# Kernel tuning notes

Hardware: AMD Instinct MI355X
Metric: run time of the kernel (lower is better)

The kernel has to match this reference:

```python
import jax, jax.numpy as jnp
import numpy as np

H = 32        # query heads
KV = 8        # key/value heads
D = 128       # head_dim
GROUPS = H // KV
THETA = 10000.0


def _rope_cos_sin(position_ids):
    # position_ids: [B, S] int
    inv_freq = 1.0 / (THETA ** (jnp.arange(0, D, 2, dtype=jnp.float32) / D))  # [D/2]
    freqs = position_ids.astype(jnp.float32)[:, :, None] * inv_freq[None, None, :]  # [B,S,D/2]
    emb = jnp.concatenate([freqs, freqs], axis=-1)  # [B,S,D]
    return jnp.cos(emb), jnp.sin(emb)


def _rotate_half(x):
    x1, x2 = jnp.split(x, 2, axis=-1)
    return jnp.concatenate([-x2, x1], axis=-1)


def _apply_rope(x, cos, sin):
    # x: [B,h,S,D]; cos/sin: [B,S,D] -> broadcast over heads
    return x * cos[:, None, :, :] + _rotate_half(x) * sin[:, None, :, :]


def setup_inputs() -> dict:
    key = jax.random.key(0)
    ks = jax.random.split(key, 8)
    B, S, Dm = 2, 2048, 4096
    scale = lambda d: 1.0 / np.sqrt(d)
    hidden_states = jax.random.normal(ks[0], (B, S, Dm), dtype=jnp.float32)
    position_ids = jnp.broadcast_to(jnp.arange(S, dtype=jnp.int32)[None, :], (B, S))
    Wq = jax.random.normal(ks[1], (Dm, H * D), dtype=jnp.float32) * scale(Dm)
    Wk = jax.random.normal(ks[2], (Dm, KV * D), dtype=jnp.float32) * scale(Dm)
    Wv = jax.random.normal(ks[3], (Dm, KV * D), dtype=jnp.float32) * scale(Dm)
    Wo = jax.random.normal(ks[4], (H * D, Dm), dtype=jnp.float32) * scale(H * D)
    # per-head shift-encoder correction weights (small init so it's a correction)
    Ws_q = jax.random.normal(ks[5], (H, D, D), dtype=jnp.float32) * (0.02 * scale(D))
    Ws_k = jax.random.normal(ks[6], (H, D, D), dtype=jnp.float32) * (0.02 * scale(D))
    return {"hidden_states": hidden_states, "position_ids": position_ids,
            "Wq": Wq, "Wk": Wk, "Wv": Wv, "Wo": Wo, "Ws_q": Ws_q, "Ws_k": Ws_k}


def reference(hidden_states, position_ids, Wq, Wk, Wv, Wo, Ws_q, Ws_k):
    B, S, Dm = hidden_states.shape
    # projections -> [B, heads, S, D]
    q = (hidden_states @ Wq).reshape(B, S, H, D).transpose(0, 2, 1, 3)
    k = (hidden_states @ Wk).reshape(B, S, KV, D).transpose(0, 2, 1, 3)
    v = (hidden_states @ Wv).reshape(B, S, KV, D).transpose(0, 2, 1, 3)
    # RoPE
    cos, sin = _rope_cos_sin(position_ids)
    q = _apply_rope(q, cos, sin)
    k = _apply_rope(k, cos, sin)
    # GQA repeat_kv: [B,KV,S,D] -> [B,H,S,D]
    k = jnp.repeat(k, GROUPS, axis=1)
    v = jnp.repeat(v, GROUPS, axis=1)
    # causal SDPA
    scores = jnp.einsum('bhqd,bhkd->bhqk', q, k) / jnp.sqrt(jnp.float32(D))
    causal = jnp.tril(jnp.ones((S, S), dtype=bool))
    scores = jnp.where(causal[None, None, :, :], scores, jnp.float32(-1e30))
    probs = jax.nn.softmax(scores, axis=-1)
    attn = jnp.einsum('bhqk,bhkd->bhqd', probs, v)  # [B,H,S,D]
    attn = attn.transpose(0, 2, 1, 3)               # [B,S,H,D]
    # shift_encoder.do_shift: per-head linear correction from rotated Q and K
    delta = jnp.einsum('bhsd,hde->bshe', q, Ws_q) + jnp.einsum('bhsd,hde->bshe', k, Ws_k)
    attn = attn + delta
    # output projection
    out = attn.reshape(B, S, H * D) @ Wo
    return out
```

## Files before the change

### kernel.cpp

```cpp
#include <hip/hip_runtime.h>
#include <cstdint>

#define DEV __device__ __forceinline__

typedef __attribute__((ext_vector_type(4))) float  f32x4;
typedef __attribute__((ext_vector_type(8))) short  s16x8;
typedef __attribute__((ext_vector_type(4))) unsigned short u16x4;
typedef __attribute__((ext_vector_type(8))) unsigned short u16x8;

constexpr int B_   = 2;
constexpr int S_   = 2048;
constexpr int DM   = 4096;
constexpr int HQ   = 32;
constexpr int KVH  = 8;
constexpr int DH   = 128;
constexpr int NQKV = 6144;

DEV unsigned short f2bf(float f) {
  union { float f; unsigned u; } c; c.f = f;
  unsigned u = c.u + 0x7FFFu + ((c.u >> 16) & 1u);
  return (unsigned short)(u >> 16);
}
DEV float bf2f(unsigned short h) {
  union { unsigned u; float f; } c; c.u = (unsigned)h << 16; return c.f;
}
DEV void gload16(const void* g, const void* l) {
  __builtin_amdgcn_global_load_lds(
      (const __attribute__((address_space(1))) unsigned int*)(uintptr_t)g,
      (__attribute__((address_space(3))) unsigned int*)(unsigned)(uintptr_t)l,
      16, 0, 0);
}
DEV f32x4 mfma16x16(s16x8 a, s16x8 b, f32x4 c) {
  return __builtin_amdgcn_mfma_f32_16x16x32_bf16(a, b, c, 0, 0, 0);
}

__global__ __launch_bounds__(256) void k_tables(const int* __restrict__ pos,
                                                float* __restrict__ ct,
                                                float* __restrict__ st) {
  int i = blockIdx.x * 256 + threadIdx.x;
  if (i >= B_ * S_ * 64) return;
  int f = i & 63, bs = i >> 6;
  float p   = (float)pos[bs];
  float inv = __builtin_amdgcn_exp2f(-(float)f * 0.20762050593048355f);
  float a   = p * inv;
  ct[i] = cosf(a);
  st[i] = sinf(a);
}

__global__ __launch_bounds__(256) void k_cvt(const float* __restrict__ in,
                                             unsigned short* __restrict__ out,
                                             int n8) {
  int i = blockIdx.x * 256 + threadIdx.x;
  if (i >= n8) return;
  const f32x4* p = (const f32x4*)in + (size_t)2 * i;
  f32x4 a = p[0], b = p[1];
  u16x8 o;
  o[0] = f2bf(a[0]); o[1] = f2bf(a[1]); o[2] = f2bf(a[2]); o[3] = f2bf(a[3]);
  o[4] = f2bf(b[0]); o[5] = f2bf(b[1]); o[6] = f2bf(b[2]); o[7] = f2bf(b[3]);
  ((u16x8*)out)[i] = o;
}

__global__ __launch_bounds__(256) void k_tconv(const float* __restrict__ in,
                                               unsigned short* __restrict__ out,
                                               int R, int C,
                                               unsigned long long ibs,
                                               unsigned long long obs) {
  __shared__ float t[64][65];
  const int r0 = blockIdx.y * 64, c0 = blockIdx.x * 64;
  const float* ib = in + (size_t)blockIdx.z * ibs;
  unsigned short* ob = out + (size_t)blockIdx.z * obs;
  const int tid = threadIdx.x, tr = tid >> 4, c4 = (tid & 15) * 4;
#pragma unroll
  for (int it = 0; it < 4; ++it) {
    int rr = it * 16 + tr;
    f32x4 v = *(const f32x4*)&ib[(size_t)(r0 + rr) * C + (c0 + c4)];
    t[rr][c4 + 0] = v[0]; t[rr][c4 + 1] = v[1];
    t[rr][c4 + 2] = v[2]; t[rr][c4 + 3] = v[3];
  }
  __syncthreads();
#pragma unroll
  for (int it = 0; it < 4; ++it) {
    int cc = it * 16 + tr;
    u16x4 o;
    o[0] = f2bf(t[c4 + 0][cc]); o[1] = f2bf(t[c4 + 1][cc]);
    o[2] = f2bf(t[c4 + 2][cc]); o[3] = f2bf(t[c4 + 3][cc]);
    *(u16x4*)&ob[(size_t)(c0 + cc) * R + (r0 + c4)] = o;
  }
}

template <int BF16OUT, int SPLIT>
__global__ __launch_bounds__(512, 2) void k_gemm256(const unsigned short* __restrict__ A,
                                                    const unsigned short* __restrict__ BT,
                                                    void* __restrict__ Cv,
                                                    unsigned short* __restrict__ Pv,
                                                    int M, int N, int K, int NBX) {
  extern __shared__ __align__(16) char L[];
  const int tid = threadIdx.x;
  const int lane = tid & 63, w = tid >> 6;
  const int g = lane >> 4, ml = lane & 15;
  const int wr = w & 1, wc = w >> 1;

  int by, bx, koff, klen, cls = 0, ksl = 0;
  if (SPLIT) {
    const int sub = (int)blockIdx.x & 255;
    const int swz = (sub & 7) * 32 + (sub >> 3);
    cls = (int)blockIdx.x >> 8;
    if (cls == 0) { by = swz >> 4; bx = swz & 15; koff = 0; klen = K; }
    else {
      ksl = swz >> 7;
      int v = swz & 127;
      by = v >> 3; bx = 16 + (v & 7);
      koff = ksl * (K >> 1); klen = K >> 1;
    }
  } else {
    const int cpx = (int)gridDim.x >> 3;
    const int swz = ((int)blockIdx.x & 7) * cpx + ((int)blockIdx.x >> 3);
    by = swz / NBX; bx = swz - by * NBX; koff = 0; klen = K;
  }
  const int bm = by * 256, bn = bx * 256;

  const int srow_l = tid >> 3;
  const int scol_e = (((tid & 7) ^ ((tid >> 3) & 7)) << 3);
  const int nk = klen >> 6;

#define STAGE(kt, hf) do {                                                        \
    if ((kt) < nk) {                                                              \
      const unsigned short* sb; char* db;                                         \
      if ((hf) < 2) { sb = A  + (size_t)(bm + (hf) * 128) * K;                    \
                      db = L + ((kt) & 1) * 32768 + (hf) * 16384; }               \
      else          { sb = BT + (size_t)(bn + ((hf) - 2) * 128) * K;              \
                      db = L + 65536 + ((kt) & 1) * 32768 + ((hf) - 2) * 16384; } \
      sb += (size_t)koff + (size_t)(kt) * 64 + scol_e;                            \
      _Pragma("unroll")                                                           \
      for (int r_ = 0; r_ < 2; ++r_)                                              \
        gload16(sb + (size_t)(r_ * 64 + srow_l) * K, db + r_ * 8192 + w * 1024);  \
    } } while (0)

  f32x4 Z = {0.f, 0.f, 0.f, 0.f};
  f32x4 acc[8][4];
#pragma unroll
  for (int i = 0; i < 8; ++i)
#pragma unroll
    for (int j = 0; j < 4; ++j) acc[i][j] = Z;
  s16x8 bfr[4][2], afr[2][2];

#define FRAG(base, row, ks)                                                       \
  ((const s16x8*)((base) + ((((row) >> 7) * 16384 + ((row) & 127) * 128 +         \
                             ((ks) * 32 + 8 * g) * 2) ^ (((row) & 7) << 4))))

#define PHASE(q, kbuf, SKT, SHF, VM) do {                                         \
    if ((q) == 0) {                                                               \
      _Pragma("unroll")                                                           \
      for (int nf = 0; nf < 4; ++nf)                                              \
        _Pragma("unroll")                                                         \
        for (int ks = 0; ks < 2; ++ks)                                            \
          bfr[nf][ks] = *FRAG(L + 65536 + (kbuf) * 32768,                         \
                              wc * 64 + nf * 16 + ml, ks);                        \
    }                                                                             \
    _Pragma("unroll")                                                             \
    for (int mm = 0; mm < 2; ++mm)                                                \
      _Pragma("unroll")                                                           \
      for (int ks = 0; ks < 2; ++ks)                                              \
        afr[mm][ks] = *FRAG(L + (kbuf) * 32768,                                   \
                            32 * (2 * (q) + mm) + 16 * wr + ml, ks);              \
    STAGE(SKT, SHF);                                                              \
    if ((VM) == 1) { asm volatile("s_waitcnt vmcnt(6)" ::: "memory"); }           \
    else if ((VM) == 2) {                                                         \
      if (last) { asm volatile("s_waitcnt vmcnt(0)" ::: "memory"); }              \
      else      { asm volatile("s_waitcnt vmcnt(6)" ::: "memory"); }              \
    } else if ((VM) == 3) {                                                       \
      if (!last) { asm volatile("s_waitcnt vmcnt(6)" ::: "memory"); }             \
    }                                                                             \
    __builtin_amdgcn_s_barrier();                                                 \
    asm volatile("s_waitcnt lgkmcnt(0)" ::: "memory");                            \
    __builtin_amdgcn_sched_barrier(0);                                            \
    __builtin_amdgcn_s_setprio(1);                                                \
    _Pragma("unroll")                                                             \
    for (int ks = 0; ks < 2; ++ks)                                                \
      _Pragma("unroll")                                                           \
      for (int mm = 0; mm < 2; ++mm)                                              \
        _Pragma("unroll")                                                         \
        for (int nf = 0; nf < 4; ++nf)                                            \
          acc[2 * (q) + mm][nf] =                                                 \
              mfma16x16(afr[mm][ks], bfr[nf][ks], acc[2 * (q) + mm][nf]);         \
    __builtin_amdgcn_s_setprio(0);                                                \
    __builtin_amdgcn_s_barrier();                                                 \
  } while (0)

  STAGE(0, 0); STAGE(0, 1); STAGE(0, 2); STAGE(0, 3);
  STAGE(1, 2); STAGE(1, 3); STAGE(1, 0);
  asm volatile("s_waitcnt vmcnt(6)" ::: "memory");
  __builtin_amdgcn_s_barrier();

  const int iters = nk >> 1;
  for (int i = 0; i < iters; ++i) {
    const int t = 2 * i;
    const bool last = (i == iters - 1);
    PHASE(0, 0, t + 1, 1, 0);
    PHASE(1, 0, t + 2, 2, 0);
    PHASE(2, 0, t + 2, 0, 0);
    PHASE(3, 0, t + 2, 3, 2);
    PHASE(0, 1, t + 2, 1, 0);
    PHASE(1, 1, t + 3, 2, 0);
    PHASE(2, 1, t + 3, 3, 0);
    PHASE(3, 1, t + 3, 0, 3);
  }
#undef PHASE
#undef FRAG
#undef STAGE

  const int row0 = bm + 16 * wr + 4 * g, col0 = bn + wc * 64 + ml;
  const bool toPart = (SPLIT && cls == 1 && ksl == 1);
#pragma unroll
  for (int m = 0; m < 8; ++m)
#pragma unroll
    for (int nf = 0; nf < 4; ++nf)
#pragma unroll
      for (int r = 0; r < 4; ++r) {
        int row = row0 + 32 * m + r;
        int col = col0 + nf * 16;
        if (BF16OUT) {
          if (toPart)
            Pv[(size_t)row * 2048 + (col - 4096)] = f2bf(acc[m][nf][r]);
          else
            ((unsigned short*)Cv)[(size_t)row * N + col] = f2bf(acc[m][nf][r]);
        } else {
          ((float*)Cv)[(size_t)row * N + col] = acc[m][nf][r];
        }
      }
}

__global__ __launch_bounds__(256) void k_rope(const unsigned short* __restrict__ qkv,
                                              const unsigned short* __restrict__ p1,
                                              const float* __restrict__ ct,
                                              const float* __restrict__ st,
                                              unsigned short* __restrict__ qr,
                                              unsigned short* __restrict__ kr) {
  const int bs = blockIdx.x;
  const int b = bs >> 11, s = bs & 2047;
  const int tid = threadIdx.x;
  const float* cr = ct + (size_t)bs * 64;
  const float* sr = st + (size_t)bs * 64;
  const unsigned short* row = qkv + (size_t)bs * NQKV;
  {
    int h = tid >> 3, d0 = (tid & 7) * 16;
    u16x8 xs  = *(const u16x8*)&row[h * 128 + d0];
    u16x8 xs2 = *(const u16x8*)&row[h * 128 + d0 + 8];
    u16x8 xp  = *(const u16x8*)&row[h * 128 + (d0 ^ 64)];
    u16x8 xp2 = *(const u16x8*)&row[h * 128 + (d0 ^ 64) + 8];
    float sg = (d0 < 64) ? -1.f : 1.f;
    int ci = d0 & 63;
    u16x8 o1, o2;
#pragma unroll
    for (int j = 0; j < 8; ++j)
      o1[j] = f2bf(bf2f(xs[j]) * cr[ci + j] + sg * bf2f(xp[j]) * sr[ci + j]);
#pragma unroll
    for (int j = 0; j < 8; ++j)
      o2[j] = f2bf(bf2f(xs2[j]) * cr[ci + 8 + j] + sg * bf2f(xp2[j]) * sr[ci + 8 + j]);
    unsigned short* dst = qr + ((size_t)(b * HQ + h) * S_ + s) * DH + d0;
    *(u16x8*)dst = o1;
    *(u16x8*)(dst + 8) = o2;
  }
  if (tid < 64) {
    int kv = tid >> 3, d0 = (tid & 7) * 16;
    const unsigned short* krow = row + HQ * DH + kv * 128;
    const unsigned short* prow = p1 + (size_t)bs * 2048 + kv * 128;
    u16x8 xs  = *(const u16x8*)&krow[d0];
    u16x8 xs2 = *(const u16x8*)&krow[d0 + 8];
    u16x8 xp  = *(const u16x8*)&krow[d0 ^ 64];
    u16x8 xp2 = *(const u16x8*)&krow[(d0 ^ 64) + 8];
    u16x8 ys  = *(const u16x8*)&prow[d0];
    u16x8 ys2 = *(const u16x8*)&prow[d0 + 8];
    u16x8 yp  = *(const u16x8*)&prow[d0 ^ 64];
    u16x8 yp2 = *(const u16x8*)&prow[(d0 ^ 64) + 8];
    float sg = (d0 < 64) ? -1.f : 1.f;
    int ci = d0 & 63;
    u16x8 o1, o2;
#pragma unroll
    for (int j = 0; j < 8; ++j)
      o1[j] = f2bf((bf2f(xs[j]) + bf2f(ys[j])) * cr[ci + j] +
                   sg * (bf2f(xp[j]) + bf2f(yp[j])) * sr[ci + j]);
#pragma unroll
    for (int j = 0; j < 8; ++j)
      o2[j] = f2bf((bf2f(xs2[j]) + bf2f(ys2[j])) * cr[ci + 8 + j] +
                   sg * (bf2f(xp2[j]) + bf2f(yp2[j])) * sr[ci + 8 + j]);
    unsigned short* dst = kr + ((size_t)(b * KVH + kv) * S_ + s) * DH + d0;
    *(u16x8*)dst = o1;
    *(u16x8*)(dst + 8) = o2;
  }
}

__global__ __launch_bounds__(256) void k_vtrans(const unsigned short* __restrict__ qkv,
                                                const unsigned short* __restrict__ p1,
                                                unsigned short* __restrict__ vt) {
  __shared__ unsigned short t[64][65];
  const int z = blockIdx.z, b = z >> 3, kv = z & 7;
  const int s0 = blockIdx.x * 64, d0 = blockIdx.y * 64;
  const int tid = threadIdx.x, tr = tid >> 4, c4 = (tid & 15) * 4;
  const unsigned short* src = qkv + (size_t)(b * S_) * NQKV + HQ * DH + KVH * DH + kv * 128;
  const unsigned short* psr = p1 + (size_t)(b * S_) * 2048 + 1024 + kv * 128;
#pragma unroll
  for (int it = 0; it < 4; ++it) {
    int s = it * 16 + tr;
    u16x4 v = *(const u16x4*)&src[(size_t)(s0 + s) * NQKV + d0 + c4];
    u16x4 q = *(const u16x4*)&psr[(size_t)(s0 + s) * 2048 + d0 + c4];
    t[s][c4 + 0] = f2bf(bf2f(v[0]) + bf2f(q[0]));
    t[s][c4 + 1] = f2bf(bf2f(v[1]) + bf2f(q[1]));
    t[s][c4 + 2] = f2bf(bf2f(v[2]) + bf2f(q[2]));
    t[s][c4 + 3] = f2bf(bf2f(v[3]) + bf2f(q[3]));
  }
  __syncthreads();
  unsigned short* dst = vt + (size_t)(b * KVH + kv) * DH * S_;
#pragma unroll
  for (int it = 0; it < 4; ++it) {
    int d = it * 16 + tr;
    u16x4 o;
    o[0] = t[c4 + 0][d]; o[1] = t[c4 + 1][d];
    o[2] = t[c4 + 2][d]; o[3] = t[c4 + 3][d];
    *(u16x4*)&dst[(size_t)(d0 + d) * S_ + s0 + c4] = o;
  }
}

__global__ __launch_bounds__(256, 2) void k_attn(const unsigned short* __restrict__ qr,
                                                 const unsigned short* __restrict__ kr,
                                                 const unsigned short* __restrict__ vt,
                                                 const unsigned short* __restrict__ wsq,
                                                 const unsigned short* __restrict__ wsk,
                                                 unsigned short* __restrict__ att) {
  const int h = blockIdx.y, b = blockIdx.z, kvh = h >> 2;
  const int tid = threadIdx.x, lane = tid & 63, w = tid >> 6;
  const int g = lane >> 4, ml = lane & 15;

  __shared__ unsigned short kvbuf[16384];
  __shared__ unsigned short pbuf[4][32 * 68];
  unsigned short* kl = kvbuf;
  unsigned short* vl = kvbuf + 8192;

  const unsigned short* Kg = kr + (size_t)(b * KVH + kvh) * S_ * DH;
  const unsigned short* Vg = vt + (size_t)(b * KVH + kvh) * DH * S_;
  const float CS = 0.12751745f;
  f32x4 Z = {0.f, 0.f, 0.f, 0.f};
  u16x8 pfk[4], pfv[4];

  for (int half = 0; half < 2; ++half) {
    const int qbx = half ? (15 - (int)blockIdx.x) : (int)blockIdx.x;
    const int qb0 = qbx * 128;
    const unsigned short* Qg = qr + ((size_t)(b * HQ + h) * S_ + qb0) * DH;

    __syncthreads();
#pragma unroll
    for (int it = 0; it < 8; ++it) {
      int c = w + 4 * it;
      int off = c * 1024 + lane * 16;
      int row = off >> 8;
      int sch = ((off >> 4) & 15) ^ (row & 7);
      gload16(Qg + (size_t)row * DH + sch * 8, (const char*)kvbuf + c * 1024);
    }
#pragma unroll
    for (int i = 0; i < 4; ++i) {
      int off = i * 4096 + tid * 16;
      pfk[i] = *(const u16x8*)((const char*)Kg + (size_t)(off >> 8) * 256 + (off & 255));
      pfv[i] = *(const u16x8*)((const char*)Vg + (size_t)(off >> 7) * 4096 + (off & 127));
    }
    __syncthreads();
    s16x8 qfr[2][4];
#pragma unroll
    for (int qf = 0; qf < 2; ++qf)
#pragma unroll
      for (int ds = 0; ds < 4; ++ds) {
        int row = 32 * w + 16 * qf + ml;
        int sch = (4 * ds + g) ^ (row & 7);
        qfr[qf][ds] = *(const s16x8*)((const char*)kvbuf + row * 256 + sch * 16);
      }
    __syncthreads();

    float mstate[2] = {-3e30f, -3e30f};
    float lstate[2] = {0.f, 0.f};
    f32x4 oacc[2][8];
#pragma unroll
    for (int i = 0; i < 2; ++i)
#pragma unroll
      for (int j = 0; j < 8; ++j) oacc[i][j] = Z;

    const int ntiles = (qb0 >> 6) + 2;

    for (int t = 0; t < ntiles; ++t) {
      const int kv0 = t * 64;
#pragma unroll
      for (int i = 0; i < 4; ++i) {
        int off = i * 4096 + tid * 16;
        int rk = off >> 8, ck = off & 255;
        *(u16x8*)((char*)kl + rk * 256 + (ck ^ ((rk & 7) << 4))) = pfk[i];
        int rv = off >> 7, cv = off & 127;
        *(u16x8*)((char*)vl + rv * 128 + (cv ^ ((rv & 7) << 4))) = pfv[i];
      }
      if (t + 1 < ntiles) {
        const int kv1 = kv0 + 64;
#pragma unroll
        for (int i = 0; i < 4; ++i) {
          int off = i * 4096 + tid * 16;
          pfk[i] = *(const u16x8*)((const char*)Kg + (size_t)(kv1 + (off >> 8)) * 256 + (off & 255));
          pfv[i] = *(const u16x8*)((const char*)Vg + (size_t)(off >> 7) * 4096 + kv1 * 2 + (off & 127));
        }
      }
      __syncthreads();

      f32x4 sacc[4][2];
#pragma unroll
      for (int i = 0; i < 4; ++i) { sacc[i][0] = Z; sacc[i][1] = Z; }
#pragma unroll
      for (int ds = 0; ds < 4; ++ds) {
        s16x8 af[4];
#pragma unroll
        for (int kf = 0; kf < 4; ++kf) {
          int row = 16 * kf + ml;
          int sch = (4 * ds + g) ^ (row & 7);
          af[kf] = *(const s16x8*)((const char*)kl + row * 256 + sch * 16);
        }
#pragma unroll
        for (int kf = 0; kf < 4; ++kf)
#pragma unroll
          for (int qf = 0; qf < 2; ++qf)
            sacc[kf][qf] = mfma16x16(af[kf], qfr[qf][ds], sacc[kf][qf]);
      }

      const int qg = qb0 + 32 * w + ml;
      const bool fullTile = (kv0 + 63 <= qb0 + 32 * w);
      float alpha[2];
      bool keep[2];
#pragma unroll
      for (int qf = 0; qf < 2; ++qf) {
        int qq = qg + 16 * qf;
        float mx = -3e30f;
        if (fullTile) {
#pragma unroll
          for (int kf = 0; kf < 4; ++kf)
#pragma unroll
            for (int r = 0; r < 4; ++r) {
              float sv = sacc[kf][qf][r] * CS;
              sacc[kf][qf][r] = sv;
              mx = fmaxf(mx, sv);
            }
        } else {
#pragma unroll
          for (int kf = 0; kf < 4; ++kf)
#pragma unroll
            for (int r = 0; r < 4; ++r) {
              float sv = sacc[kf][qf][r] * CS;
              int kk = kv0 + 16 * kf + 4 * g + r;
              sv = (kk <= qq) ? sv : -3e30f;
              sacc[kf][qf][r] = sv;
              mx = fmaxf(mx, sv);
            }
        }
        mx = fmaxf(mx, __shfl_xor(mx, 16));
        mx = fmaxf(mx, __shfl_xor(mx, 32));
        keep[qf] = __all(mx - mstate[qf] <= 8.0f);
        float mn, al;
        if (keep[qf]) { mn = mstate[qf]; al = 1.0f; }
        else {
          mn = fmaxf(mstate[qf], mx);
          al = __builtin_amdgcn_exp2f(mstate[qf] - mn);
          mstate[qf] = mn;
        }
        alpha[qf] = al;
        float ls = 0.f;
#pragma unroll
        for (int kf = 0; kf < 4; ++kf) {
          u16x4 pk;
#pragma unroll
          for (int r = 0; r < 4; ++r) {
            float p = __builtin_amdgcn_exp2f(sacc[kf][qf][r] - mn);
            ls += p;
            pk[r] = f2bf(p);
          }
          *(u16x4*)&pbuf[w][(16 * qf + ml) * 68 + 16 * kf + 4 * g] = pk;
        }
        ls += __shfl_xor(ls, 16);
        ls += __shfl_xor(ls, 32);
        lstate[qf] = lstate[qf] * alpha[qf] + ls;
      }
      if (!(keep[0] && keep[1])) {
#pragma unroll
        for (int mf = 0; mf < 2; ++mf)
#pragma unroll
          for (int r = 0; r < 4; ++r) {
            float a = __shfl(alpha[mf], (lane & 48) | (4 * g + r));
#pragma unroll
            for (int nf = 0; nf < 8; ++nf) oacc[mf][nf][r] *= a;
          }
      }
#pragma unroll
      for (int ks = 0; ks < 2; ++ks) {
        s16x8 pa[2];
#pragma unroll
        for (int mf = 0; mf < 2; ++mf) {
          const unsigned short* pr = &pbuf[w][(16 * mf + ml) * 68 + 32 * ks + 8 * g];
          u16x4 lo = *(const u16x4*)pr;
          u16x4 hi = *(const u16x4*)(pr + 4);
          pa[mf] = (s16x8)__builtin_shufflevector(lo, hi, 0, 1, 2, 3, 4, 5, 6, 7);
        }
#pragma unroll
        for (int nf = 0; nf < 8; ++nf) {
          int row = 16 * nf + ml;
          int sch = (4 * ks + g) ^ (row & 7);
          s16x8 bv = *(const s16x8*)((const char*)vl + row * 128 + sch * 16);
#pragma unroll
          for (int mf = 0; mf < 2; ++mf)
            oacc[mf][nf] = mfma16x16(pa[mf], bv, oacc[mf][nf]);
        }
      }
      __syncthreads();
    }

#pragma unroll
    for (int mf = 0; mf < 2; ++mf)
#pragma unroll
      for (int r = 0; r < 4; ++r) {
        float li = __shfl(lstate[mf], (lane & 48) | (4 * g + r));
        float inv = 1.0f / li;
#pragma unroll
        for (int nf = 0; nf < 8; ++nf) oacc[mf][nf][r] *= inv;
      }

    s16x8 kfr[2][4];
#pragma unroll
    for (int it = 0; it < 8; ++it) {
      int c = w + 4 * it;
      int off = c * 1024 + lane * 16;
      int row = off >> 8;
      int sch = ((off >> 4) & 15) ^ (row & 7);
      gload16(Kg + (size_t)(qb0 + row) * DH + sch * 8, (const char*)kvbuf + c * 1024);
    }
    __syncthreads();
#pragma unroll
    for (int qf = 0; qf < 2; ++qf)
#pragma unroll
      for (int ds = 0; ds < 4; ++ds) {
        int row = 32 * w + 16 * qf + ml;
        int sch = (4 * ds + g) ^ (row & 7);
        kfr[qf][ds] = *(const s16x8*)((const char*)kvbuf + row * 256 + sch * 16);
      }

#pragma unroll
    for (int pass = 0; pass < 2; ++pass) {
      const unsigned short* Wg = (pass == 0 ? wsq : wsk) + (size_t)h * DH * DH;
      __syncthreads();
#pragma unroll
      for (int it = 0; it < 8; ++it) {
        int c = w + 4 * it;
        int off = c * 1024 + lane * 16;
        int row = off >> 8;
        int sch = ((off >> 4) & 15) ^ (row & 7);
        gload16(Wg + (size_t)row * DH + sch * 8, (const char*)kvbuf + c * 1024);
      }
      __syncthreads();
#pragma unroll
      for (int ds = 0; ds < 4; ++ds)
#pragma unroll
        for (int nf = 0; nf < 8; ++nf) {
          int row = 16 * nf + ml;
          int sch = (4 * ds + g) ^ (row & 7);
          s16x8 wf = *(const s16x8*)((const char*)kvbuf + row * 256 + sch * 16);
#pragma unroll
          for (int qf = 0; qf < 2; ++qf)
            oacc[qf][nf] = mfma16x16(pass == 0 ? qfr[qf][ds] : kfr[qf][ds],
                                     wf, oacc[qf][nf]);
        }
    }

#pragma unroll
    for (int mf = 0; mf < 2; ++mf)
#pragma unroll
      for (int r = 0; r < 4; ++r) {
        int rowg = b * S_ + qb0 + 32 * w + 16 * mf + 4 * g + r;
        size_t base = (size_t)rowg * (HQ * DH) + h * DH;
#pragma unroll
        for (int nf = 0; nf < 8; ++nf)
          att[base + 16 * nf + ml] = f2bf(oacc[mf][nf][r]);
      }
  }
}

extern "C" void kernel_launch(void* const* d_in, const int* in_sizes, int n_in,
                              void* d_out, int out_size, void* d_ws, size_t ws_size,
                              hipStream_t stream) {
  const float* hidden = (const float*)d_in[0];
  const int*   pos    = (const int*)d_in[1];
  const float* Wq     = (const float*)d_in[2];
  const float* Wk     = (const float*)d_in[3];
  const float* Wv     = (const float*)d_in[4];
  const float* Wo     = (const float*)d_in[5];
  const float* Wsq    = (const float*)d_in[6];
  const float* Wsk    = (const float*)d_in[7];

  char* ws = (char*)d_ws;
  unsigned short* XB    = (unsigned short*)(ws + 0);
  unsigned short* WQKVT = (unsigned short*)(ws + 33554432);
  unsigned short* WOT   = (unsigned short*)(ws + 83886080);
  unsigned short* P1    = WOT;
  unsigned short* WSQT  = (unsigned short*)(ws + 117440512);
  unsigned short* WSKT  = (unsigned short*)(ws + 118489088);
  float*          CT    = (float*)(ws + 119537664);
  float*          ST    = (float*)(ws + 120586240);
  unsigned short* QKV   = (unsigned short*)(ws + 121634816);
  unsigned short* QR    = (unsigned short*)(ws + 171966464);
  unsigned short* KR    = (unsigned short*)(ws + 205520896);
  unsigned short* VT    = (unsigned short*)(ws + 213909504);
  unsigned short* ATT   = (unsigned short*)(ws + 222298112);

  k_tables<<<1024, 256, 0, stream>>>(pos, CT, ST);
  k_cvt<<<8192, 256, 0, stream>>>(hidden, XB, 2097152);
  k_tconv<<<dim3(64, 64, 1), 256, 0, stream>>>(Wq, WQKVT, 4096, 4096, 0, 0);
  k_tconv<<<dim3(16, 64, 1), 256, 0, stream>>>(Wk, WQKVT + (size_t)4096 * 4096, 4096, 1024, 0, 0);
  k_tconv<<<dim3(16, 64, 1), 256, 0, stream>>>(Wv, WQKVT + (size_t)5120 * 4096, 4096, 1024, 0, 0);
  k_tconv<<<dim3(2, 2, 32), 256, 0, stream>>>(Wsq, WSQT, 128, 128, 16384, 16384);
  k_tconv<<<dim3(2, 2, 32), 256, 0, stream>>>(Wsk, WSKT, 128, 128, 16384, 16384);
  k_gemm256<1, 1><<<dim3(512), 512, 131072, stream>>>(XB, WQKVT, QKV, P1,
                                                      4096, 6144, 4096, 0);
  k_rope<<<4096, 256, 0, stream>>>(QKV, P1, CT, ST, QR, KR);
  k_vtrans<<<dim3(32, 2, 16), 256, 0, stream>>>(QKV, P1, VT);
  k_tconv<<<dim3(64, 64, 1), 256, 0, stream>>>(Wo, WOT, 4096, 4096, 0, 0);
  k_attn<<<dim3(8, 32, 2), 256, 0, stream>>>(QR, KR, VT, WSQT, WSKT, ATT);
  k_gemm256<0, 0><<<dim3(256), 512, 131072, stream>>>(ATT, WOT, d_out, nullptr,
                                                      4096, 4096, 4096, 16);
}
```

Baseline: 535.9 us.

## Double-buffer LDS fragment reads to prefetch next phase during MFMA

Restructures the GEMM main loop so the A/B fragment loads from shared memory for the next phase are issued right after the current phase's MFMAs, using double-buffered fragment registers. The last iteration is peeled so the final wait counts are static. The aim is to hide LDS read latency behind matrix math. The extra fragment registers raise register pressure and could reduce occupancy.

Result: slower. 899.7 us (+67.9%).

```diff
diff --git a/kernel.cpp b/kernel.cpp
--- a/kernel.cpp
+++ b/kernel.cpp
@@ -142,35 +142,33 @@
   for (int i = 0; i < 8; ++i)
 #pragma unroll
     for (int j = 0; j < 4; ++j) acc[i][j] = Z;
-  s16x8 bfr[4][2], afr[2][2];
+  s16x8 afr[2][2][2], bfr[2][4][2];
 
 #define FRAG(base, row, ks)                                                       \
   ((const s16x8*)((base) + ((((row) >> 7) * 16384 + ((row) & 127) * 128 +         \
                              ((ks) * 32 + 8 * g) * 2) ^ (((row) & 7) << 4))))
 
-#define PHASE(q, kbuf, SKT, SHF, VM) do {                                         \
-    if ((q) == 0) {                                                               \
+#define RDNEXT(NQ, NKBUF) do {                                                    \
+    if ((NQ) == 0) {                                                              \
       _Pragma("unroll")                                                           \
       for (int nf = 0; nf < 4; ++nf)                                              \
         _Pragma("unroll")                                                         \
         for (int ks = 0; ks < 2; ++ks)                                            \
-          bfr[nf][ks] = *FRAG(L + 65536 + (kbuf) * 32768,                         \
-                              wc * 64 + nf * 16 + ml, ks);                        \
+          bfr[NKBUF][nf][ks] = *FRAG(L + 65536 + (NKBUF) * 32768,                 \
+                                     wc * 64 + nf * 16 + ml, ks);                 \
     }                                                                             \
     _Pragma("unroll")                                                             \
     for (int mm = 0; mm < 2; ++mm)                                                \
       _Pragma("unroll")                                                           \
       for (int ks = 0; ks < 2; ++ks)                                              \
-        afr[mm][ks] = *FRAG(L + (kbuf) * 32768,                                   \
-                            32 * (2 * (q) + mm) + 16 * wr + ml, ks);              \
+        afr[(NQ) & 1][mm][ks] = *FRAG(L + (NKBUF) * 32768,                        \
+                                      32 * (2 * (NQ) + mm) + 16 * wr + ml, ks);   \
+  } while (0)
+
+#define PHASE(q, kbuf, SKT, SHF, VM, NQ, NKBUF) do {                              \
     STAGE(SKT, SHF);                                                              \
     if ((VM) == 1) { asm volatile("s_waitcnt vmcnt(6)" ::: "memory"); }           \
-    else if ((VM) == 2) {                                                         \
-      if (last) { asm volatile("s_waitcnt vmcnt(0)" ::: "memory"); }              \
-      else      { asm volatile("s_waitcnt vmcnt(6)" ::: "memory"); }              \
-    } else if ((VM) == 3) {                                                       \
-      if (!last) { asm volatile("s_waitcnt vmcnt(6)" ::: "memory"); }             \
-    }                                                                             \
+    else if ((VM) == 2) { asm volatile("s_waitcnt vmcnt(0)" ::: "memory"); }      \
     __builtin_amdgcn_s_barrier();                                                 \
     asm volatile("s_waitcnt lgkmcnt(0)" ::: "memory");                            \
     __builtin_amdgcn_sched_barrier(0);                                            \
@@ -181,9 +179,11 @@
       for (int mm = 0; mm < 2; ++mm)                                              \
         _Pragma("unroll")                                                         \
         for (int nf = 0; nf < 4; ++nf)                                            \
-          acc[2 * (q) + mm][nf] =                                                 \
-              mfma16x16(afr[mm][ks], bfr[nf][ks], acc[2 * (q) + mm][nf]);         \
+          acc[2 * (q) + mm][nf] = mfma16x16(afr[(q) & 1][mm][ks],                 \
+                                            bfr[kbuf][nf][ks],                    \
+                                            acc[2 * (q) + mm][nf]);               \
     __builtin_amdgcn_s_setprio(0);                                                \
+    RDNEXT(NQ, NKBUF);                                                            \
     __builtin_amdgcn_s_barrier();                                                 \
   } while (0)
 
@@ -191,21 +191,33 @@
   STAGE(1, 2); STAGE(1, 3); STAGE(1, 0);
   asm volatile("s_waitcnt vmcnt(6)" ::: "memory");
   __builtin_amdgcn_s_barrier();
+  RDNEXT(0, 0);
 
   const int iters = nk >> 1;
-  for (int i = 0; i < iters; ++i) {
+  for (int i = 0; i < iters - 1; ++i) {
     const int t = 2 * i;
-    const bool last = (i == iters - 1);
-    PHASE(0, 0, t + 1, 1, 0);
-    PHASE(1, 0, t + 2, 2, 0);
-    PHASE(2, 0, t + 2, 0, 0);
-    PHASE(3, 0, t + 2, 3, 2);
-    PHASE(0, 1, t + 2, 1, 0);
-    PHASE(1, 1, t + 3, 2, 0);
-    PHASE(2, 1, t + 3, 3, 0);
-    PHASE(3, 1, t + 3, 0, 3);
+    PHASE(0, 0, t + 1, 1, 0, 1, 0);
+    PHASE(1, 0, t + 2, 2, 0, 2, 0);
+    PHASE(2, 0, t + 2, 0, 0, 3, 0);
+    PHASE(3, 0, t + 2, 3, 1, 0, 1);
+    PHASE(0, 1, t + 2, 1, 0, 1, 1);
+    PHASE(1, 1, t + 3, 2, 0, 2, 1);
+    PHASE(2, 1, t + 3, 3, 0, 3, 1);
+    PHASE(3, 1, t + 3, 0, 1, 0, 0);
+  }
+  {
+    const int t = nk - 2;
+    PHASE(0, 0, t + 1, 1, 0, 1, 0);
+    PHASE(1, 0, t + 2, 2, 0, 2, 0);
+    PHASE(2, 0, t + 2, 0, 0, 3, 0);
+    PHASE(3, 0, t + 2, 3, 2, 0, 1);
+    PHASE(0, 1, t + 2, 1, 0, 1, 1);
+    PHASE(1, 1, t + 3, 2, 0, 2, 1);
+    PHASE(2, 1, t + 3, 3, 0, 3, 1);
+    PHASE(3, 1, t + 3, 0, 0, 0, 0);
   }
 #undef PHASE
+#undef RDNEXT
 #undef FRAG
 #undef STAGE
 
```
